# Kernel tuning notes

Measured on AMD Instinct MI355X. Metric: run time of the kernel, lower is better.

The kernel has to match this reference:

```python
import jax, jax.numpy as jnp
import numpy as np

BATCH = 8192
N_BANDS = 2000
TARGET = 500
FIRST_HIDDEN = 50
LEAKY_SLOPE = 0.01  # torch LeakyReLU default


def _tridiag_solve(lower, diag, upper, rhs):
    """Thomas algorithm. lower/upper: (n-1,), diag: (n,), rhs: (n, B). Returns (n, B)."""
    dt = rhs.dtype
    up = jnp.concatenate([upper, jnp.zeros((1,), dt)])   # (n,)
    lo = jnp.concatenate([jnp.zeros((1,), dt), lower])   # (n,)

    def fwd(carry, inp):
        cp_prev, dp_prev = carry
        d_i, u_i, l_i, r_i = inp
        m = d_i - l_i * cp_prev
        cp = u_i / m
        dp = (r_i - l_i * dp_prev) / m
        return (cp, dp), (cp, dp)

    init = (jnp.zeros((), dt), jnp.zeros(rhs.shape[1:], dt))
    _, (cps, dps) = jax.lax.scan(fwd, init, (diag, up, lo, rhs))

    def bwd(x_next, inp):
        cp, dp = inp
        x = dp - cp * x_next
        return x, x

    _, xs = jax.lax.scan(bwd, jnp.zeros(rhs.shape[1:], dt), (cps, dps), reverse=True)
    return xs


def natural_cubic_spline_coeffs(times, path):
    """times: (n,), path: (B, n) -> (a, b, two_c, three_d), each (B, n-1)."""
    h = times[1:] - times[:-1]            # (n-1,)
    hr = 1.0 / h
    hr2 = hr * hr
    diffs3 = 3.0 * (path[:, 1:] - path[:, :-1])   # (B, n-1)
    diffs6 = 2.0 * diffs3
    pds = diffs3 * hr2                             # (B, n-1)
    n = path.shape[1]
    diag = (jnp.zeros((n,), path.dtype).at[:-1].set(hr).at[1:].add(hr)) * 2.0
    rhs = jnp.zeros_like(path).at[:, :-1].set(pds).at[:, 1:].add(pds)  # (B, n)
    kd = _tridiag_solve(hr, diag, hr, rhs.T).T     # knot derivatives (B, n)
    a = path[:, :-1]
    b = kd[:, :-1]
    two_c = (diffs6 * hr - 4.0 * kd[:, :-1] - 2.0 * kd[:, 1:]) * hr
    three_d = (-diffs6 * hr + 3.0 * (kd[:, :-1] + kd[:, 1:])) * hr2
    return a, b, two_c, three_d


def spline_evaluate(times, coeffs, t):
    """Evaluate at points t: (T,). Returns (B, T)."""
    a, b, two_c, three_d = coeffs
    idx = jnp.clip(jnp.searchsorted(times, t, side='left') - 1, 0, times.shape[0] - 2)
    frac = t - times[idx]                  # (T,)
    inner = 0.5 * two_c[:, idx] + three_d[:, idx] * frac / 3.0
    inner = b[:, idx] + inner * frac
    return a[:, idx] + inner * frac


def leaky_relu(x):
    return jnp.where(x >= 0, x, LEAKY_SLOPE * x)


def setup_inputs() -> dict:
    key = jax.random.key(0)
    ks = jax.random.split(key, 8)
    return {
        'x': jax.random.uniform(ks[0], (BATCH, N_BANDS), dtype=jnp.float32),
        'raw_index': jax.random.normal(ks[1], (TARGET,), dtype=jnp.float32),
        'W1': jax.random.normal(ks[2], (TARGET, FIRST_HIDDEN), dtype=jnp.float32) * 0.05,
        'b1': jax.random.normal(ks[3], (FIRST_HIDDEN,), dtype=jnp.float32) * 0.05,
        'W2': jax.random.normal(ks[4], (FIRST_HIDDEN, 10), dtype=jnp.float32) * 0.1,
        'b2': jax.random.normal(ks[5], (10,), dtype=jnp.float32) * 0.1,
        'W3': jax.random.normal(ks[6], (10, 1), dtype=jnp.float32) * 0.1,
        'b3': jax.random.normal(ks[7], (1,), dtype=jnp.float32) * 0.1,
    }


def reference(x, raw_index, W1, b1, W2, b2, W3, b3):
    # x: (B, n_bands). Spline is fit along the band axis with knots linspace(0,1,n_bands).
    times = jnp.linspace(0.0, 1.0, x.shape[1]).astype(x.dtype)
    coeffs = natural_cubic_spline_coeffs(times, x)
    # Each BandIndex machine evaluates the spline at sigmoid(raw_index_i) -> batched over all i.
    t_eval = jax.nn.sigmoid(raw_index)             # (T,)
    outputs = spline_evaluate(times, coeffs, t_eval)  # (B, T)
    h = leaky_relu(outputs @ W1 + b1)
    h = leaky_relu(h @ W2 + b2)
    soc_hat = (h @ W3 + b3).reshape(-1)            # (B,)
    return soc_hat
```

## Files before the change

### kernel.cpp

```cpp
#include <hip/hip_runtime.h>

#define NB 2000
#define BATCH 8192
#define NT 500
#define NH1 50
#define NH2 10
#define HRc 1999.0f
#define STEPc (1.0f/1999.0f)
#define LP 520

typedef __attribute__((ext_vector_type(8))) short short8;
typedef __attribute__((ext_vector_type(4))) float f32x4;

__device__ __forceinline__ float b2f(unsigned short u) {
    return __uint_as_float(((unsigned int)u) << 16);
}
__device__ __forceinline__ unsigned short f2b(float f) {
    unsigned int u = __float_as_uint(f);
    return (unsigned short)((u + 0x7FFFu + ((u >> 16) & 1u)) >> 16);
}
__device__ __forceinline__ float ldv(const void* p, int i, int flag) {
    return flag ? b2f(((const unsigned short*)p)[i]) : ((const float*)p)[i];
}
__device__ __forceinline__ int wave_detect(const void* x) {
    const unsigned char* xb = (const unsigned char*)x;
    int lane = threadIdx.x & 63;
    int pred = xb[4 * lane + 1] > 0x3F;
    unsigned long long m = __ballot(pred);
    return (__popcll(m) > 4) ? 0 : 1;
}

__global__ __launch_bounds__(64, 1) void p1_stencil(
        const void* __restrict__ xdet, const void* __restrict__ raw_index,
        float* __restrict__ S_coef, int* __restrict__ S_base) {
    __shared__ float cp_tab[64];
    __shared__ float sc[2];
    int tid = threadIdx.x;
    int flag = wave_detect(xdet);
    if (tid == 0) {
        double cp = 0.5;
        cp_tab[0] = 0.5f;
        for (int i = 1; i < 64; ++i) { cp = 1.0 / (4.0 - cp); cp_tab[i] = (float)cp; }
        sc[0] = (float)cp;
        sc[1] = (float)(1.0 / (2.0 - cp));
    }
    __syncthreads();
    int t = blockIdx.x * 64 + tid;
    if (t >= NT) return;
    float c_inf = sc[0], w_last = sc[1];

    float coef_rel[34];
    #pragma unroll
    for (int k = 0; k < 34; ++k) coef_rel[k] = 0.0f;

    float r = ldv(raw_index, t, flag);
    float v = 1.0f / (1.0f + expf(-r));
    int lo = 0, hi = NB;
    while (lo < hi) {
        int mid = (lo + hi) >> 1;
        float tm = (float)mid * STEPc;
        if (tm < v) lo = mid + 1; else hi = mid;
    }
    int idx = lo - 1;
    idx = idx < 0 ? 0 : (idx > NB - 2 ? NB - 2 : idx);
    float f = v - (float)idx * STEPc;
    float u = f * HRc;
    float A = 1.0f + u * u * (2.0f * u - 3.0f);
    float B = u * u * (3.0f - 2.0f * u);
    float C = f * (1.0f - u) * (1.0f - u);
    float D = f * u * (u - 1.0f);

    const float g3 = 3.0f * HRc * HRc;
    const float invhr = 1.0f / HRc;

    #pragma unroll
    for (int row = 0; row < 2; ++row) {
        int j = idx + row;
        float scale = row ? D : C;
        float z[35];
        #pragma unroll
        for (int q = 0; q < 35; ++q) z[q] = 0.0f;
        float w0 = (j <= NB - 2) ? ((j < 64) ? cp_tab[j] : c_inf) : w_last;
        z[17] = w0 * invhr;
        #pragma unroll
        for (int s = 1; s <= 17; ++s) {
            int m = j + s;
            float wm;
            if (m <= NB - 2)      wm = (m < 64) ? cp_tab[m] : c_inf;
            else if (m == NB - 1) wm = w_last;
            else                  wm = 0.0f;
            z[17 + s] = -wm * z[17 + s - 1];
        }
        #pragma unroll
        for (int s = 16; s >= -17; --s) {
            int m = j + s;
            float cpv;
            if (m >= NB - 1 || m < 0) cpv = 0.0f;
            else                      cpv = (m < 64) ? cp_tab[m] : c_inf;
            z[17 + s] = z[17 + s] - cpv * z[17 + s + 1];
        }
        #pragma unroll
        for (int s = -16; s <= 16; ++s) {
            int m = j + s;
            float gv = 0.0f;
            if (m >= 1)      gv += z[17 + s - 1];
            if (m <= NB - 2) gv -= z[17 + s + 1];
            if (m == NB - 1) gv += z[17 + s];
            if (m == 0)      gv -= z[17 + s];
            gv *= g3;
            bool valid = (m >= 0) && (m <= NB - 1);
            coef_rel[s + row + 16] += valid ? scale * gv : 0.0f;
        }
    }
    coef_rel[16] += A;
    coef_rel[17] += B;

    #pragma unroll
    for (int j = 0; j < 34; ++j) S_coef[t * 34 + j] = coef_rel[j];
    S_base[t] = idx;
}

__global__ __launch_bounds__(256) void m_build2(
        const void* __restrict__ xdet, const void* __restrict__ W1,
        const float* __restrict__ S_coef, const int* __restrict__ S_base,
        unsigned int* __restrict__ MB) {
    __shared__ int sb[NT];
    __shared__ float red0[4][64];
    __shared__ float red1[4][64];
    int tid = threadIdx.x;
    int flag = wave_detect(xdet);
    for (int i = tid; i < NT; i += 256) sb[i] = S_base[i];
    __syncthreads();
    int wv = tid >> 6;
    int h = tid & 63;
    int hh = h < NH1 ? h : NH1 - 1;
    int k2 = blockIdx.x;
    int k0 = 2 * k2;
    float acc0 = 0.0f, acc1 = 0.0f;
    if (k0 < NB) {
        int t0 = wv * 125, t1 = t0 + 125;
        #pragma unroll 4
        for (int t = t0; t < t1; ++t) {
            int idx = sb[t];
            int rel0 = k0 - idx + 16;
            if (rel0 >= -1 && rel0 < 34) {
                float w1v = ldv(W1, t * NH1 + hh, flag);
                if (rel0 >= 0)  acc0 += S_coef[t * 34 + rel0] * w1v;
                if (rel0 < 33)  acc1 += S_coef[t * 34 + rel0 + 1] * w1v;
            }
        }
    }
    red0[wv][h] = acc0;
    red1[wv][h] = acc1;
    __syncthreads();
    if (tid < 64) {
        float a0 = ((red0[0][tid] + red0[1][tid]) + red0[2][tid]) + red0[3][tid];
        float a1 = ((red1[0][tid] + red1[1][tid]) + red1[2][tid]) + red1[3][tid];
        int hh2 = tid;
        bool ok = (hh2 < NH1) && (k0 < NB);
        unsigned int lo16 = ok ? (unsigned int)f2b(a0) : 0u;
        unsigned int hi16 = ok ? (unsigned int)f2b(a1) : 0u;
        int kt = k0 >> 5;
        int kr = k0 & 31;
        int gg = kr >> 3;
        int j  = kr & 7;
        int ht = hh2 >> 4;
        int lt = gg * 16 + (hh2 & 15);
        MB[(((kt * 4 + ht) * 64 + lt) << 2) + (j >> 1)] = lo16 | (hi16 << 16);
    }
}

__global__ __launch_bounds__(512, 4) void g_fused(
        const void* __restrict__ x, const unsigned int* __restrict__ MB,
        const void* __restrict__ b1, const void* __restrict__ W2,
        const void* __restrict__ b2, const void* __restrict__ W3,
        const void* __restrict__ b3, void* __restrict__ out) {
    __shared__ __align__(16) unsigned short lx[2][16 * LP];
    __shared__ float red[8][16][68];
    __shared__ float Wmlp[NH1 * NH2 + NH1 + NH2 + NH2 + 1];

    int tid = threadIdx.x;
    int flag = wave_detect(x);

    for (int i = tid; i < NH1 * NH2; i += 512) Wmlp[i] = ldv(W2, i, flag);
    if (tid < NH1) Wmlp[500 + tid] = ldv(b1, tid, flag);
    if (tid < NH2) Wmlp[550 + tid] = ldv(b2, tid, flag);
    if (tid < NH2) Wmlp[560 + tid] = ldv(W3, tid, flag);
    if (tid == 0)  Wmlp[570] = ldv(b3, 0, flag);

    int lane = tid & 63;
    int c16  = tid & 15;
    int g    = (tid >> 4) & 3;
    int w    = tid >> 6;
    int srow = tid >> 5;
    int soff = tid & 31;
    int r0   = blockIdx.x * 16;
    const unsigned short* xs = (const unsigned short*)x;
    const float*          xf = (const float*)x;
    size_t crow = (size_t)(r0 + srow) * NB;

    f32x4 acc[4];
    #pragma unroll
    for (int ht = 0; ht < 4; ++ht) acc[ht] = (f32x4){0.f, 0.f, 0.f, 0.f};

    union AU { uint4 u; short8 s; };
    const uint4* mb4 = (const uint4*)MB;

    if (flag) {
        uint4 pf[8];
        #pragma unroll
        for (int c = 0; c < 4; ++c) {
            int gk0 = c * 512 + soff * 8;
            int gk1 = gk0 + 256;
            pf[2 * c]     = (gk0 + 8 <= NB) ? *(const uint4*)(xs + crow + gk0)
                                            : make_uint4(0u, 0u, 0u, 0u);
            pf[2 * c + 1] = (gk1 + 8 <= NB) ? *(const uint4*)(xs + crow + gk1)
                                            : make_uint4(0u, 0u, 0u, 0u);
        }
        *(uint4*)&lx[0][srow * LP + soff * 8]       = pf[0];
        *(uint4*)&lx[0][srow * LP + soff * 8 + 256] = pf[1];

        int cur = 0;
        #pragma unroll
        for (int c = 0; c < 4; ++c) {
            __syncthreads();
            #pragma unroll
            for (int dk = 0; dk < 2; ++dk) {
                int ktl = 2 * w + dk;
                AU a;
                a.u = *(const uint4*)&lx[cur][c16 * LP + ktl * 32 + g * 8];
                int kt = c * 16 + ktl;
                #pragma unroll
                for (int ht = 0; ht < 4; ++ht) {
                    AU b; b.u = mb4[(kt * 4 + ht) * 64 + lane];
                    acc[ht] = __builtin_amdgcn_mfma_f32_16x16x32_bf16(a.s, b.s, acc[ht], 0, 0, 0);
                }
            }
            if (c < 3) {
                *(uint4*)&lx[cur ^ 1][srow * LP + soff * 8]       = pf[2 * (c + 1)];
                *(uint4*)&lx[cur ^ 1][srow * LP + soff * 8 + 256] = pf[2 * (c + 1) + 1];
            }
            __syncthreads();
            cur ^= 1;
        }
    } else {
        #define LDSEGF(dst, gk) do {                                          \
            int _gk = (gk);                                                   \
            if (_gk + 8 <= NB) {                                              \
                float4 _v0 = *(const float4*)(xf + crow + _gk);               \
                float4 _v1 = *(const float4*)(xf + crow + _gk + 4);           \
                (dst).x = (unsigned)f2b(_v0.x) | ((unsigned)f2b(_v0.y) << 16); \
                (dst).y = (unsigned)f2b(_v0.z) | ((unsigned)f2b(_v0.w) << 16); \
                (dst).z = (unsigned)f2b(_v1.x) | ((unsigned)f2b(_v1.y) << 16); \
                (dst).w = (unsigned)f2b(_v1.z) | ((unsigned)f2b(_v1.w) << 16); \
            } else {                                                          \
                (dst) = make_uint4(0u, 0u, 0u, 0u);                           \
            }                                                                 \
        } while (0)
        {
            uint4 p0, p1;
            LDSEGF(p0, soff * 8);
            LDSEGF(p1, soff * 8 + 256);
            *(uint4*)&lx[0][srow * LP + soff * 8]       = p0;
            *(uint4*)&lx[0][srow * LP + soff * 8 + 256] = p1;
        }
        int cur = 0;
        #pragma unroll
        for (int c = 0; c < 4; ++c) {
            __syncthreads();
            uint4 s0 = make_uint4(0u,0u,0u,0u), s1 = make_uint4(0u,0u,0u,0u);
            if (c < 3) {
                LDSEGF(s0, (c + 1) * 512 + soff * 8);
                LDSEGF(s1, (c + 1) * 512 + soff * 8 + 256);
            }
            #pragma unroll
            for (int dk = 0; dk < 2; ++dk) {
                int ktl = 2 * w + dk;
                AU a;
                a.u = *(const uint4*)&lx[cur][c16 * LP + ktl * 32 + g * 8];
                int kt = c * 16 + ktl;
                #pragma unroll
                for (int ht = 0; ht < 4; ++ht) {
                    AU b; b.u = mb4[(kt * 4 + ht) * 64 + lane];
                    acc[ht] = __builtin_amdgcn_mfma_f32_16x16x32_bf16(a.s, b.s, acc[ht], 0, 0, 0);
                }
            }
            if (c < 3) {
                *(uint4*)&lx[cur ^ 1][srow * LP + soff * 8]       = s0;
                *(uint4*)&lx[cur ^ 1][srow * LP + soff * 8 + 256] = s1;
            }
            __syncthreads();
            cur ^= 1;
        }
        #undef LDSEGF
    }

    #pragma unroll
    for (int ht = 0; ht < 4; ++ht)
        #pragma unroll
        for (int r = 0; r < 4; ++r)
            red[w][g * 4 + r][ht * 16 + c16] = acc[ht][r];
    __syncthreads();

    #pragma unroll
    for (int ii = 0; ii < 2; ++ii) {
        int idx = tid + ii * 512;
        int row = idx >> 6, h = idx & 63;
        float s = 0.0f;
        #pragma unroll
        for (int w2 = 0; w2 < 8; ++w2) s += red[w2][row][h];
        red[0][row][h] = s;
    }
    __syncthreads();

    if (tid < 16) {
        float h1v[NH1];
        #pragma unroll
        for (int h = 0; h < NH1; ++h) {
            float vv = red[0][tid][h] + Wmlp[500 + h];
            h1v[h] = vv >= 0.0f ? vv : 0.01f * vv;
        }
        float o = Wmlp[570];
        for (int j = 0; j < NH2; ++j) {
            float a2 = Wmlp[550 + j];
            #pragma unroll
            for (int h = 0; h < NH1; ++h)
                a2 = fmaf(h1v[h], Wmlp[h * NH2 + j], a2);
            a2 = a2 >= 0.0f ? a2 : 0.01f * a2;
            o = fmaf(a2, Wmlp[560 + j], o);
        }
        int b = r0 + tid;
        if (flag) ((unsigned short*)out)[b] = f2b(o);
        else      ((float*)out)[b] = o;
    }
}

extern "C" void kernel_launch(void* const* d_in, const int* in_sizes, int n_in,
                              void* d_out, int out_size, void* d_ws, size_t ws_size,
                              hipStream_t stream) {
    const void* x   = d_in[0];
    const void* raw = d_in[1];
    const void* W1  = d_in[2];
    const void* b1  = d_in[3];
    const void* W2  = d_in[4];
    const void* b2  = d_in[5];
    const void* W3  = d_in[6];
    const void* b3  = d_in[7];

    float* w      = (float*)d_ws;
    int*   S_base = (int*)w;
    float* S_coef = w + 512;
    unsigned int* MB = (unsigned int*)(w + 17512);

    p1_stencil<<<8, 64, 0, stream>>>(x, raw, S_coef, S_base);
    m_build2<<<1024, 256, 0, stream>>>(x, W1, S_coef, S_base, MB);
    g_fused<<<512, 512, 0, stream>>>(x, MB, b1, W2, b2, W3, b3, d_out);
}
```

Baseline: 136.9 us.

## Fuse spline stencil computation into W1 matrix-build kernel, recomputing per block

Removes the separate single-wave stencil kernel and its global S_coef/S_base buffers. Each m_build block now recomputes the sigmoid, binary search and tridiagonal inverse stencil for every relevant eval point, staging z through shared memory. This drops one launch and the serial dependency on a tiny 8-block kernel. In exchange it adds a lot of redundant per-block arithmetic, each of the 64 lanes in a wave repeats the same stencil, and zW is written and read by every lane without a barrier.

```diff
diff --git a/kernel.cpp b/kernel.cpp
--- a/kernel.cpp
+++ b/kernel.cpp
@@ -30,13 +30,19 @@
     return (__popcll(m) > 4) ? 0 : 1;
 }
 
-__global__ __launch_bounds__(64, 1) void p1_stencil(
-        const void* __restrict__ xdet, const void* __restrict__ raw_index,
-        float* __restrict__ S_coef, int* __restrict__ S_base) {
+__global__ __launch_bounds__(256) void m_build3(
+        const void* __restrict__ x, const void* __restrict__ raw_index,
+        const void* __restrict__ W1, unsigned int* __restrict__ MB) {
+    __shared__ int   sbS[NT];
+    __shared__ float vS[NT];
+    __shared__ float red0[4][64];
+    __shared__ float red1[4][64];
+    __shared__ float zW[4][40];
     __shared__ float cp_tab[64];
     __shared__ float sc[2];
+
     int tid = threadIdx.x;
-    int flag = wave_detect(xdet);
+    int flag = wave_detect(x);
     if (tid == 0) {
         double cp = 0.5;
         cp_tab[0] = 0.5f;
@@ -45,108 +51,114 @@
         sc[1] = (float)(1.0 / (2.0 - cp));
     }
     __syncthreads();
-    int t = blockIdx.x * 64 + tid;
-    if (t >= NT) return;
     float c_inf = sc[0], w_last = sc[1];
 
-    float coef_rel[34];
-    #pragma unroll
-    for (int k = 0; k < 34; ++k) coef_rel[k] = 0.0f;
-
-    float r = ldv(raw_index, t, flag);
-    float v = 1.0f / (1.0f + expf(-r));
-    int lo = 0, hi = NB;
-    while (lo < hi) {
-        int mid = (lo + hi) >> 1;
-        float tm = (float)mid * STEPc;
-        if (tm < v) lo = mid + 1; else hi = mid;
-    }
-    int idx = lo - 1;
-    idx = idx < 0 ? 0 : (idx > NB - 2 ? NB - 2 : idx);
-    float f = v - (float)idx * STEPc;
-    float u = f * HRc;
-    float A = 1.0f + u * u * (2.0f * u - 3.0f);
-    float B = u * u * (3.0f - 2.0f * u);
-    float C = f * (1.0f - u) * (1.0f - u);
-    float D = f * u * (u - 1.0f);
-
-    const float g3 = 3.0f * HRc * HRc;
-    const float invhr = 1.0f / HRc;
-
-    #pragma unroll
-    for (int row = 0; row < 2; ++row) {
-        int j = idx + row;
-        float scale = row ? D : C;
-        float z[35];
-        #pragma unroll
-        for (int q = 0; q < 35; ++q) z[q] = 0.0f;
-        float w0 = (j <= NB - 2) ? ((j < 64) ? cp_tab[j] : c_inf) : w_last;
-        z[17] = w0 * invhr;
-        #pragma unroll
-        for (int s = 1; s <= 17; ++s) {
-            int m = j + s;
-            float wm;
-            if (m <= NB - 2)      wm = (m < 64) ? cp_tab[m] : c_inf;
-            else if (m == NB - 1) wm = w_last;
-            else                  wm = 0.0f;
-            z[17 + s] = -wm * z[17 + s - 1];
-        }
-        #pragma unroll
-        for (int s = 16; s >= -17; --s) {
-            int m = j + s;
-            float cpv;
-            if (m >= NB - 1 || m < 0) cpv = 0.0f;
-            else                      cpv = (m < 64) ? cp_tab[m] : c_inf;
-            z[17 + s] = z[17 + s] - cpv * z[17 + s + 1];
-        }
-        #pragma unroll
-        for (int s = -16; s <= 16; ++s) {
-            int m = j + s;
-            float gv = 0.0f;
-            if (m >= 1)      gv += z[17 + s - 1];
-            if (m <= NB - 2) gv -= z[17 + s + 1];
-            if (m == NB - 1) gv += z[17 + s];
-            if (m == 0)      gv -= z[17 + s];
-            gv *= g3;
-            bool valid = (m >= 0) && (m <= NB - 1);
-            coef_rel[s + row + 16] += valid ? scale * gv : 0.0f;
-        }
-    }
-    coef_rel[16] += A;
-    coef_rel[17] += B;
-
-    #pragma unroll
-    for (int j = 0; j < 34; ++j) S_coef[t * 34 + j] = coef_rel[j];
-    S_base[t] = idx;
-}
-
-__global__ __launch_bounds__(256) void m_build2(
-        const void* __restrict__ xdet, const void* __restrict__ W1,
-        const float* __restrict__ S_coef, const int* __restrict__ S_base,
-        unsigned int* __restrict__ MB) {
-    __shared__ int sb[NT];
-    __shared__ float red0[4][64];
-    __shared__ float red1[4][64];
-    int tid = threadIdx.x;
-    int flag = wave_detect(xdet);
-    for (int i = tid; i < NT; i += 256) sb[i] = S_base[i];
-    __syncthreads();
+    for (int rep = 0; rep < 2; ++rep) {
+        int t = tid + rep * 256;
+        if (t < NT) {
+            float r = ldv(raw_index, t, flag);
+            float v = 1.0f / (1.0f + expf(-r));
+            int lo = 0, hi = NB;
+            while (lo < hi) {
+                int mid = (lo + hi) >> 1;
+                float tm = (float)mid * STEPc;
+                if (tm < v) lo = mid + 1; else hi = mid;
+            }
+            int idx = lo - 1;
+            idx = idx < 0 ? 0 : (idx > NB - 2 ? NB - 2 : idx);
+            sbS[t] = idx;
+            vS[t]  = v;
+        }
+    }
+    __syncthreads();
+
     int wv = tid >> 6;
     int h = tid & 63;
     int hh = h < NH1 ? h : NH1 - 1;
     int k2 = blockIdx.x;
     int k0 = 2 * k2;
+    const float g3 = 3.0f * HRc * HRc;
+    const float invhr = 1.0f / HRc;
     float acc0 = 0.0f, acc1 = 0.0f;
     if (k0 < NB) {
         int t0 = wv * 125, t1 = t0 + 125;
-        #pragma unroll 4
         for (int t = t0; t < t1; ++t) {
-            int idx = sb[t];
+            int idx = sbS[t];
             int rel0 = k0 - idx + 16;
             if (rel0 >= -1 && rel0 < 34) {
+                float v = vS[t];
+                float f = v - (float)idx * STEPc;
+                float u = f * HRc;
+                float A = 1.0f + u * u * (2.0f * u - 3.0f);
+                float B = u * u * (3.0f - 2.0f * u);
+                float C = f * (1.0f - u) * (1.0f - u);
+                float D = f * u * (u - 1.0f);
+
+                float c0 = 0.0f, c1 = 0.0f;
+                #pragma unroll
+                for (int row = 0; row < 2; ++row) {
+                    int j = idx + row;
+                    float scale = row ? D : C;
+                    float z[35];
+                    #pragma unroll
+                    for (int q = 0; q < 35; ++q) z[q] = 0.0f;
+                    float w0 = (j <= NB - 2) ? ((j < 64) ? cp_tab[j] : c_inf) : w_last;
+                    z[17] = w0 * invhr;
+                    #pragma unroll
+                    for (int s = 1; s <= 17; ++s) {
+                        int m = j + s;
+                        float wm;
+                        if (m <= NB - 2)      wm = (m < 64) ? cp_tab[m] : c_inf;
+                        else if (m == NB - 1) wm = w_last;
+                        else                  wm = 0.0f;
+                        z[17 + s] = -wm * z[17 + s - 1];
+                    }
+                    #pragma unroll
+                    for (int s = 16; s >= -17; --s) {
+                        int m = j + s;
+                        float cpv;
+                        if (m >= NB - 1 || m < 0) cpv = 0.0f;
+                        else                      cpv = (m < 64) ? cp_tab[m] : c_inf;
+                        z[17 + s] = z[17 + s] - cpv * z[17 + s + 1];
+                    }
+                    #pragma unroll
+                    for (int q = 0; q < 35; ++q) zW[wv][q] = z[q];
+
+                    {
+                        int s0 = rel0 - 16 - row;
+                        if (rel0 >= 0 && s0 >= -16 && s0 <= 16) {
+                            int m = j + s0;
+                            float gv = 0.0f;
+                            if (m >= 1)      gv += zW[wv][17 + s0 - 1];
+                            if (m <= NB - 2) gv -= zW[wv][17 + s0 + 1];
+                            if (m == NB - 1) gv += zW[wv][17 + s0];
+                            if (m == 0)      gv -= zW[wv][17 + s0];
+                            gv *= g3;
+                            bool valid = (m >= 0) && (m <= NB - 1);
+                            c0 += valid ? scale * gv : 0.0f;
+                        }
+                        int s1 = s0 + 1;
+                        if (rel0 < 33 && s1 >= -16 && s1 <= 16) {
+                            int m = j + s1;
+                            float gv = 0.0f;
+                            if (m >= 1)      gv += zW[wv][17 + s1 - 1];
+                            if (m <= NB - 2) gv -= zW[wv][17 + s1 + 1];
+                            if (m == NB - 1) gv += zW[wv][17 + s1];
+                            if (m == 0)      gv -= zW[wv][17 + s1];
+                            gv *= g3;
+                            bool valid = (m >= 0) && (m <= NB - 1);
+                            c1 += valid ? scale * gv : 0.0f;
+                        }
+                    }
+                }
+                if (rel0 == 16)     c0 += A;
+                if (rel0 == 17)     c0 += B;
+                if (rel0 + 1 == 16) c1 += A;
+                if (rel0 + 1 == 17) c1 += B;
+
                 float w1v = ldv(W1, t * NH1 + hh, flag);
-                if (rel0 >= 0)  acc0 += S_coef[t * 34 + rel0] * w1v;
-                if (rel0 < 33)  acc1 += S_coef[t * 34 + rel0 + 1] * w1v;
+                if (rel0 >= 0)  acc0 += c0 * w1v;
+                if (rel0 < 33)  acc1 += c1 * w1v;
             }
         }
     }
@@ -347,12 +359,9 @@
     const void* W3  = d_in[6];
     const void* b3  = d_in[7];
 
-    float* w      = (float*)d_ws;
-    int*   S_base = (int*)w;
-    float* S_coef = w + 512;
+    float* w = (float*)d_ws;
     unsigned int* MB = (unsigned int*)(w + 17512);
 
-    p1_stencil<<<8, 64, 0, stream>>>(x, raw, S_coef, S_base);
-    m_build2<<<1024, 256, 0, stream>>>(x, W1, S_coef, S_base, MB);
+    m_build3<<<1024, 256, 0, stream>>>(x, raw, W1, MB);
     g_fused<<<512, 512, 0, stream>>>(x, MB, b1, W2, b2, W3, b3, d_out);
 }
```

Result: slower. 176.6 us (+29.0%).
